# Performance work log

Measured on AMD Instinct MI355X. Metric: run time of the kernel, lower is better.

Reference implementation:

```python
import jax, jax.numpy as jnp
import numpy as np
import math

N_HEADS = 16
EMBED = 1024
D_KEY = EMBED // N_HEADS
B, S = 2, 2048
NEG = -1000000000.0


def setup_inputs() -> dict:
    key = jax.random.key(0)
    ks = jax.random.split(key, 7)
    scale = 1.0 / math.sqrt(EMBED)
    x = jax.random.normal(ks[0], (B, S, EMBED), dtype=jnp.float32)
    Wq_w = jax.random.uniform(ks[1], (EMBED, EMBED), jnp.float32, -scale, scale)
    Wq_b = jax.random.uniform(ks[2], (EMBED,), jnp.float32, -scale, scale)
    Wk_w = jax.random.uniform(ks[3], (EMBED, EMBED), jnp.float32, -scale, scale)
    Wk_b = jax.random.uniform(ks[4], (EMBED,), jnp.float32, -scale, scale)
    Wv_w = jax.random.uniform(ks[5], (EMBED, EMBED), jnp.float32, -scale, scale)
    Wv_b = jax.random.uniform(ks[6], (EMBED,), jnp.float32, -scale, scale)
    return {"x": x, "Wq_w": Wq_w, "Wq_b": Wq_b, "Wk_w": Wk_w, "Wk_b": Wk_b,
            "Wv_w": Wv_w, "Wv_b": Wv_b, "is_masked": 1}


def reference(x, Wq_w, Wq_b, Wk_w, Wk_b, Wv_w, Wv_b, is_masked):
    b, s, e = x.shape
    # nn.Linear: y = x @ W.T + b
    q = x @ Wq_w.T + Wq_b
    k = x @ Wk_w.T + Wk_b
    v = x @ Wv_w.T + Wv_b
    # [B, H, S, Dk]
    q = q.reshape(b, s, N_HEADS, D_KEY).transpose(0, 2, 1, 3)
    k = k.reshape(b, s, N_HEADS, D_KEY).transpose(0, 2, 1, 3)
    v = v.reshape(b, s, N_HEADS, D_KEY).transpose(0, 2, 1, 3)
    scores = jnp.einsum("bhqd,bhkd->bhqk", q, k) / math.sqrt(D_KEY)
    # non-standard mask: keep positions where score != padding (0)
    mask = scores != 0.0
    if is_masked:
        causal = jnp.tril(jnp.ones((1, s, s), dtype=bool))  # broadcasts over B,H
        mask = causal[None] & mask  # [1,1,S,S] & [B,H,S,S]
    scores = jnp.where(mask, scores, NEG)
    probs = jax.nn.softmax(scores, axis=-1)
    out = jnp.einsum("bhqk,bhkd->bhqd", probs, v)
    return out.transpose(0, 2, 1, 3).reshape(b, s, e)
```

## Files before the change

kernel.cpp:

```cpp
#include <hip/hip_runtime.h>

#define B_SZ   2
#define NH     16
#define S_LEN  2048
#define DK     64
#define EMB    1024
#define M_TOT  (B_SZ * S_LEN)
#define KT     64

typedef float          f32x4  __attribute__((ext_vector_type(4)));
typedef float          f32x16 __attribute__((ext_vector_type(16)));
typedef unsigned int   u32x4  __attribute__((ext_vector_type(4)));
typedef unsigned short u16x8  __attribute__((ext_vector_type(8)));
typedef unsigned short u16x4  __attribute__((ext_vector_type(4)));
typedef __bf16         bf16x8 __attribute__((ext_vector_type(8)));

static __device__ __forceinline__ f32x4 mfma16(u16x8 a, u16x8 b, f32x4 c) {
    return __builtin_amdgcn_mfma_f32_16x16x32_bf16(
        __builtin_bit_cast(bf16x8, a), __builtin_bit_cast(bf16x8, b), c, 0, 0, 0);
}
static __device__ __forceinline__ f32x16 mfma32(u16x8 a, u16x8 b, f32x16 c) {
    return __builtin_amdgcn_mfma_f32_32x32x16_bf16(
        __builtin_bit_cast(bf16x8, a), __builtin_bit_cast(bf16x8, b), c, 0, 0, 0);
}

static __device__ __forceinline__ unsigned short f2bf(float f) {
    unsigned int u = __builtin_bit_cast(unsigned int, f);
    u = (u + 0x7FFFu + ((u >> 16) & 1u)) >> 16;
    return (unsigned short)u;
}

static __device__ __forceinline__ float exp2_hw(float x) {
    float r; asm("v_exp_f32 %0, %1" : "=v"(r) : "v"(x)); return r;
}

#define GLDS16(g, l)  __builtin_amdgcn_global_load_lds(                      \
    (const void __attribute__((address_space(1)))*)(g),                      \
    (void __attribute__((address_space(3)))*)(l), 16, 0, 0)

__global__ __launch_bounds__(256) void cvt_kernel(
    const float* __restrict__ x,  const float* __restrict__ wq,
    const float* __restrict__ wk, const float* __restrict__ wv,
    unsigned short* __restrict__ xb,  unsigned short* __restrict__ wqb,
    unsigned short* __restrict__ wkb, unsigned short* __restrict__ wvb)
{
    long gid = (long)blockIdx.x * 256 + threadIdx.x;
    long e = gid * 4;
    const float* src; unsigned short* dst; long off;
    if      (e < 4194304L) { src = x;  dst = xb;  off = e; }
    else if (e < 5242880L) { src = wq; dst = wqb; off = e - 4194304L; }
    else if (e < 6291456L) { src = wk; dst = wkb; off = e - 5242880L; }
    else                   { src = wv; dst = wvb; off = e - 6291456L; }
    f32x4 v = *(const f32x4*)(src + off);
    u16x4 u;
    u[0] = f2bf(v[0]); u[1] = f2bf(v[1]); u[2] = f2bf(v[2]); u[3] = f2bf(v[3]);
    *(u16x4*)(dst + off) = u;
}

#define BM 128
#define BN 128
#define BK 64

__global__ __launch_bounds__(256) void qkv_gemm(
    const unsigned short* __restrict__ xb,
    const unsigned short* __restrict__ wb,
    const float* __restrict__ bq, const float* __restrict__ bk,
    const float* __restrict__ bv,
    unsigned short* __restrict__ qkv)
{
    const int tid  = threadIdx.x;
    const int lane = tid & 63;
    const int wid  = tid >> 6;
    const int wm   = wid >> 1, wn = wid & 1;
    const int n0   = blockIdx.x * BN;
    const int m0   = blockIdx.y * BM;
    const int mat  = blockIdx.z;

    const unsigned short* wmat = wb + (size_t)mat * (1024 * 1024);
    const float* bias = (mat == 0) ? bq : ((mat == 1) ? bk : bv);
    unsigned short* dst = qkv + (size_t)mat * ((size_t)M_TOT * EMB);

    __shared__ __align__(16) unsigned short Al[BM * 64];
    __shared__ __align__(16) unsigned short Bl[BN * 64];

    f32x4 acc[4][4];
#pragma unroll
    for (int i = 0; i < 4; ++i)
#pragma unroll
        for (int j = 0; j < 4; ++j)
            acc[i][j] = (f32x4){0.f, 0.f, 0.f, 0.f};

    const int wrow = wid * 32;
    const int lrow = lane >> 3;
    const int lcol = ((lane & 7) ^ lrow) * 8;
    const int l15  = lane & 15;
    const int sl0 = (((lane >> 4))     ^ (l15 & 7)) * 8;
    const int sl1 = ((4 + (lane >> 4)) ^ (l15 & 7)) * 8;

    for (int k0 = 0; k0 < EMB; k0 += BK) {
        const unsigned short* ga = xb   + (size_t)(m0 + wrow + lrow) * EMB + k0 + lcol;
        const unsigned short* gb = wmat + (size_t)(n0 + wrow + lrow) * EMB + k0 + lcol;
#pragma unroll
        for (int j = 0; j < 4; ++j) {
            GLDS16(ga + (size_t)j * 8 * EMB, &Al[(wrow + j * 8) * 64]);
            GLDS16(gb + (size_t)j * 8 * EMB, &Bl[(wrow + j * 8) * 64]);
        }
        __syncthreads();

#pragma unroll
        for (int kk = 0; kk < 2; ++kk) {
            const int sl = kk ? sl1 : sl0;
            u16x8 a[4], b[4];
#pragma unroll
            for (int i = 0; i < 4; ++i)
                a[i] = *(const u16x8*)&Al[(wm * 64 + i * 16 + l15) * 64 + sl];
#pragma unroll
            for (int j = 0; j < 4; ++j)
                b[j] = *(const u16x8*)&Bl[(wn * 64 + j * 16 + l15) * 64 + sl];
#pragma unroll
            for (int i = 0; i < 4; ++i)
#pragma unroll
                for (int j = 0; j < 4; ++j)
                    acc[i][j] = mfma16(a[i], b[j], acc[i][j]);
        }
        __syncthreads();
    }

#pragma unroll
    for (int j = 0; j < 4; ++j) {
        int n = n0 + wn * 64 + j * 16 + l15;
        float bvv = bias[n];
        int h = n >> 6, d = n & 63;
#pragma unroll
        for (int i = 0; i < 4; ++i) {
#pragma unroll
            for (int r = 0; r < 4; ++r) {
                int m = m0 + wm * 64 + i * 16 + ((lane >> 4) << 2) + r;
                int bb = m >> 11, s = m & 2047;
                dst[((size_t)((bb * NH + h) * S_LEN + s)) * DK + d] =
                    f2bf(acc[i][j][r] + bvv);
            }
        }
    }
}

__global__ __launch_bounds__(512) void attn_kernel(
    const unsigned short* __restrict__ Q,
    const unsigned short* __restrict__ K,
    const unsigned short* __restrict__ V,
    const int* __restrict__ mskp,
    float* __restrict__ out)
{
    const int tid = threadIdx.x, lane = tid & 63, wid = tid >> 6;
    const int grp = wid >> 2, qw = wid & 3;
    const int l31 = lane & 31, H = lane >> 5;
    const int bh = blockIdx.x;
    const int h  = bh & 15, b = bh >> 4;
    const int y  = blockIdx.y;
    const int qt = (y < 8) ? y : 23 - y;
    const int q0 = qt * 128;
    const size_t hoff = ((size_t)(b * NH + h)) * S_LEN * DK;
    const unsigned short* Qh = Q + hoff;
    const unsigned short* Kh = K + hoff;
    const unsigned short* Vh = V + hoff;
    const int msk = *mskp;
    const int ntiles = msk ? (2 * qt + 2) : (S_LEN / KT);
    const int niter  = ntiles >> 1;

    __shared__ __align__(16) unsigned short Kl[2][64 * 64];
    __shared__ __align__(16) unsigned short Vt[2][64 * 64];
    __shared__ float MLbuf[512];
    unsigned short* Kg = Kl[grp];
    unsigned short* Vg = Vt[grp];

    const int qrow = q0 + qw * 32 + l31;
    u16x8 qf[4];
#pragma unroll
    for (int ks = 0; ks < 4; ++ks)
        qf[ks] = *(const u16x8*)(Qh + (size_t)qrow * DK + ks * 16 + H * 8);

    f32x16 o0, o1;
#pragma unroll
    for (int i = 0; i < 16; ++i) { o0[i] = 0.f; o1[i] = 0.f; }
    float mx = -1e30f, lsum = 0.f;

    const int gt  = tid & 255;
    const int sr0 = gt >> 3, sc8 = gt & 7, sr1 = sr0 + 32;
    const int kwo0 = sr0 * 64 + ((sc8 ^ (sr0 & 7)) << 3);
    const int kwo1 = sr1 * 64 + ((sc8 ^ (sr1 & 7)) << 3);
    const int vwo0 = (((sr0 >> 3) ^ sc8) << 3) + (sr0 & 7);
    const int vwo1 = (((sr1 >> 3) ^ sc8) << 3) + (sr1 & 7);

    u16x8 kr[2], vr[2];
    {
        const unsigned short* K0 = Kh + (size_t)grp * KT * DK;
        const unsigned short* V0 = Vh + (size_t)grp * KT * DK;
        kr[0] = *(const u16x8*)(K0 + (size_t)sr0 * DK + sc8 * 8);
        vr[0] = *(const u16x8*)(V0 + (size_t)sr0 * DK + sc8 * 8);
        kr[1] = *(const u16x8*)(K0 + (size_t)sr1 * DK + sc8 * 8);
        vr[1] = *(const u16x8*)(V0 + (size_t)sr1 * DK + sc8 * 8);
    }

    const int qmin = q0 + qw * 32;
    const int dsw0 = l31 >> 3, dsw1 = 4 + (l31 >> 3);
    const int rsw  = l31 & 7;
    const float SC2 = 0.125f * 1.4426950408889634f;

    for (int it = 0; it < niter; ++it) {
        const int kt = 2 * it + grp;
        __syncthreads();
        *(u16x8*)&Kg[kwo0] = kr[0];
        *(u16x8*)&Kg[kwo1] = kr[1];
#pragma unroll
        for (int e = 0; e < 8; ++e) {
            Vg[(sc8 * 8 + e) * 64 + vwo0] = vr[0][e];
            Vg[(sc8 * 8 + e) * 64 + vwo1] = vr[1][e];
        }
        __syncthreads();

        if (it + 1 < niter) {
            const unsigned short* Kn = Kh + (size_t)(kt + 2) * KT * DK;
            const unsigned short* Vn = Vh + (size_t)(kt + 2) * KT * DK;
            kr[0] = *(const u16x8*)(Kn + (size_t)sr0 * DK + sc8 * 8);
            vr[0] = *(const u16x8*)(Vn + (size_t)sr0 * DK + sc8 * 8);
            kr[1] = *(const u16x8*)(Kn + (size_t)sr1 * DK + sc8 * 8);
            vr[1] = *(const u16x8*)(Vn + (size_t)sr1 * DK + sc8 * 8);
        }

        if (msk && kt * KT > qmin + 31) continue;

        f32x16 st0, st1;
#pragma unroll
        for (int i = 0; i < 16; ++i) { st0[i] = 0.f; st1[i] = 0.f; }
        __builtin_amdgcn_s_setprio(1);
#pragma unroll
        for (int ks = 0; ks < 4; ++ks) {
            const int g = (((ks << 1) + H) ^ rsw) << 3;
            u16x8 kf0 = *(const u16x8*)&Kg[l31 * 64 + g];
            u16x8 kf1 = *(const u16x8*)&Kg[(32 + l31) * 64 + g];
            st0 = mfma32(kf0, qf[ks], st0);
            st1 = mfma32(kf1, qf[ks], st1);
        }
        __builtin_amdgcn_s_setprio(0);

        const bool needmask = msk && (kt * KT + 63 > qrow);
        float p[32];
#pragma unroll
        for (int r = 0; r < 16; ++r) {
            const int krow = (r & 3) + 8 * (r >> 2) + 4 * H;
            float v0 = st0[r] * SC2;
            float v1 = st1[r] * SC2;
            if (needmask) {
                if (kt * KT + krow > qrow)      v0 = -1e30f;
                if (kt * KT + 32 + krow > qrow) v1 = -1e30f;
            }
            p[r] = v0; p[16 + r] = v1;
        }

        float t8[8];
#pragma unroll
        for (int i = 0; i < 8; ++i)
            t8[i] = fmaxf(fmaxf(p[i], p[i + 8]), fmaxf(p[i + 16], p[i + 24]));
#pragma unroll
        for (int i = 0; i < 4; ++i) t8[i] = fmaxf(t8[i], t8[i + 4]);
        float mt = fmaxf(fmaxf(t8[0], t8[1]), fmaxf(t8[2], t8[3]));
        mt = fmaxf(mt, __shfl_xor(mt, 32, 64));

        if (!__all(mt <= mx + 11.54f)) {
            const float mn = fmaxf(mx, mt);
            const float al = exp2_hw(mx - mn);
            mx = mn;
            lsum *= al;
#pragma unroll
            for (int i = 0; i < 16; ++i) { o0[i] *= al; o1[i] *= al; }
        }

        float s8[8];
#pragma unroll
        for (int i = 0; i < 8; ++i) s8[i] = 0.f;
#pragma unroll
        for (int r = 0; r < 32; ++r) {
            p[r] = exp2_hw(p[r] - mx);
            s8[r & 7] += p[r];
        }
        float ls = ((s8[0] + s8[1]) + (s8[2] + s8[3])) +
                   ((s8[4] + s8[5]) + (s8[6] + s8[7]));
        ls += __shfl_xor(ls, 32, 64);
        lsum += ls;

        __builtin_amdgcn_s_setprio(1);
#pragma unroll
        for (int ks = 0; ks < 4; ++ks) {
            const int bb = ks * 8;
            unsigned int wa, wb2, wc, wd;
            asm("v_cvt_pk_bf16_f32 %0, %1, %2" : "=v"(wa)  : "v"(p[bb + 0]), "v"(p[bb + 1]));
            asm("v_cvt_pk_bf16_f32 %0, %1, %2" : "=v"(wb2) : "v"(p[bb + 2]), "v"(p[bb + 3]));
            asm("v_cvt_pk_bf16_f32 %0, %1, %2" : "=v"(wc)  : "v"(p[bb + 4]), "v"(p[bb + 5]));
            asm("v_cvt_pk_bf16_f32 %0, %1, %2" : "=v"(wd)  : "v"(p[bb + 6]), "v"(p[bb + 7]));
            asm volatile("v_permlane32_swap_b32 %0, %1" : "+v"(wa),  "+v"(wc));
            asm volatile("v_permlane32_swap_b32 %0, %1" : "+v"(wb2), "+v"(wd));
            u32x4 wv; wv[0] = wa; wv[1] = wb2; wv[2] = wc; wv[3] = wd;
            const u16x8 pb = __builtin_bit_cast(u16x8, wv);
            const int kg = (ks << 1) + H;
            u16x8 vf0 = *(const u16x8*)&Vg[l31 * 64        + ((kg ^ dsw0) << 3)];
            u16x8 vf1 = *(const u16x8*)&Vg[(32 + l31) * 64 + ((kg ^ dsw1) << 3)];
            o0 = mfma32(vf0, pb, o0);
            o1 = mfma32(vf1, pb, o1);
        }
        __builtin_amdgcn_s_setprio(0);
    }

    const int idx = qw * 64 + lane;
    float* MO = (idx < 128) ? ((float*)Kl + idx * 32)
                            : ((float*)Vt + (idx - 128) * 32);
    __syncthreads();
    if (grp == 1) {
#pragma unroll
        for (int i = 0; i < 16; ++i) {
            MO[(i + idx) & 31]      = o0[i];
            MO[(16 + i + idx) & 31] = o1[i];
        }
        MLbuf[idx * 2]     = mx;
        MLbuf[idx * 2 + 1] = lsum;
    }
    __syncthreads();
    if (grp == 0) {
        const float m2 = MLbuf[idx * 2], l2 = MLbuf[idx * 2 + 1];
        const float mn = fmaxf(mx, m2);
        const float ea = exp2_hw(mx - mn);
        const float eb = exp2_hw(m2 - mn);
        const float inv = 1.f / (lsum * ea + l2 * eb);
        float* orow = out + ((size_t)(b * S_LEN) + qrow) * EMB + h * DK;
#pragma unroll
        for (int g = 0; g < 4; ++g) {
            f32x4 w0, w1;
#pragma unroll
            for (int i = 0; i < 4; ++i) {
                w0[i] = (o0[4 * g + i] * ea + MO[(4 * g + i + idx) & 31] * eb) * inv;
                w1[i] = (o1[4 * g + i] * ea + MO[(16 + 4 * g + i + idx) & 31] * eb) * inv;
            }
            *(f32x4*)&orow[8 * g + 4 * H]      = w0;
            *(f32x4*)&orow[32 + 8 * g + 4 * H] = w1;
        }
    }
}

extern "C" void kernel_launch(void* const* d_in, const int* in_sizes, int n_in,
                              void* d_out, int out_size, void* d_ws, size_t ws_size,
                              hipStream_t stream)
{
    const float* x  = (const float*)d_in[0];
    const float* wq = (const float*)d_in[1];
    const float* bq = (const float*)d_in[2];
    const float* wk = (const float*)d_in[3];
    const float* bk = (const float*)d_in[4];
    const float* wv = (const float*)d_in[5];
    const float* bv = (const float*)d_in[6];
    const int* msk  = (const int*)d_in[7];
    float* out = (float*)d_out;

    unsigned short* xb  = (unsigned short*)d_ws;
    unsigned short* wb  = xb + (size_t)M_TOT * EMB;
    unsigned short* qkv = wb + (size_t)3 * 1024 * 1024;

    cvt_kernel<<<7168, 256, 0, stream>>>(x, wq, wk, wv,
                                         xb, wb, wb + 1024 * 1024, wb + 2 * 1024 * 1024);
    qkv_gemm<<<dim3(8, 32, 3), 256, 0, stream>>>(xb, wb, bq, bk, bv, qkv);
    attn_kernel<<<dim3(32, 16, 1), 512, 0, stream>>>(
        qkv, qkv + (size_t)M_TOT * EMB, qkv + (size_t)2 * M_TOT * EMB, msk, out);
}
```

Before: 95.98 us.

## Double-buffer K/V LDS tiles and compute row sums via MFMA with ones

Doubles the LDS buffers for K and V so that the next tile is written into the alternate buffer while the current one is consumed. This removes one of the two block barriers per iteration. The softmax row sum is now accumulated by an extra MFMA that multiplies a ones vector with the bf16 probabilities, replacing the scalar add tree and cross-lane shuffle. In exchange, LDS use doubles, which may lower occupancy, and each iteration issues four extra MFMAs. The row sum is also taken from bf16-rounded probabilities, which changes its numerics slightly.

```diff
diff --git a/kernel.cpp b/kernel.cpp
--- a/kernel.cpp
+++ b/kernel.cpp
@@ -167,11 +167,9 @@
     const int ntiles = msk ? (2 * qt + 2) : (S_LEN / KT);
     const int niter  = ntiles >> 1;
 
-    __shared__ __align__(16) unsigned short Kl[2][64 * 64];
-    __shared__ __align__(16) unsigned short Vt[2][64 * 64];
+    __shared__ __align__(16) unsigned short Kl[2][2][64 * 64];
+    __shared__ __align__(16) unsigned short Vt[2][2][64 * 64];
     __shared__ float MLbuf[512];
-    unsigned short* Kg = Kl[grp];
-    unsigned short* Vg = Vt[grp];
 
     const int qrow = q0 + qw * 32 + l31;
     u16x8 qf[4];
@@ -179,10 +177,14 @@
     for (int ks = 0; ks < 4; ++ks)
         qf[ks] = *(const u16x8*)(Qh + (size_t)qrow * DK + ks * 16 + H * 8);
 
-    f32x16 o0, o1;
-#pragma unroll
-    for (int i = 0; i < 16; ++i) { o0[i] = 0.f; o1[i] = 0.f; }
-    float mx = -1e30f, lsum = 0.f;
+    u16x8 ones1;
+#pragma unroll
+    for (int i = 0; i < 8; ++i) ones1[i] = 0x3F80;
+
+    f32x16 o0, o1, lacc;
+#pragma unroll
+    for (int i = 0; i < 16; ++i) { o0[i] = 0.f; o1[i] = 0.f; lacc[i] = 0.f; }
+    float mx = -1e30f;
 
     const int gt  = tid & 255;
     const int sr0 = gt >> 3, sc8 = gt & 7, sr1 = sr0 + 32;
@@ -190,6 +192,11 @@
     const int kwo1 = sr1 * 64 + ((sc8 ^ (sr1 & 7)) << 3);
     const int vwo0 = (((sr0 >> 3) ^ sc8) << 3) + (sr0 & 7);
     const int vwo1 = (((sr1 >> 3) ^ sc8) << 3) + (sr1 & 7);
+
+    const int qmin = q0 + qw * 32;
+    const int dsw0 = l31 >> 3, dsw1 = 4 + (l31 >> 3);
+    const int rsw  = l31 & 7;
+    const float SC2 = 0.125f * 1.4426950408889634f;
 
     u16x8 kr[2], vr[2];
     {
@@ -199,16 +206,8 @@
         vr[0] = *(const u16x8*)(V0 + (size_t)sr0 * DK + sc8 * 8);
         kr[1] = *(const u16x8*)(K0 + (size_t)sr1 * DK + sc8 * 8);
         vr[1] = *(const u16x8*)(V0 + (size_t)sr1 * DK + sc8 * 8);
-    }
-
-    const int qmin = q0 + qw * 32;
-    const int dsw0 = l31 >> 3, dsw1 = 4 + (l31 >> 3);
-    const int rsw  = l31 & 7;
-    const float SC2 = 0.125f * 1.4426950408889634f;
-
-    for (int it = 0; it < niter; ++it) {
-        const int kt = 2 * it + grp;
-        __syncthreads();
+        unsigned short* Kg = Kl[grp][0];
+        unsigned short* Vg = Vt[grp][0];
         *(u16x8*)&Kg[kwo0] = kr[0];
         *(u16x8*)&Kg[kwo1] = kr[1];
 #pragma unroll
@@ -216,104 +215,124 @@
             Vg[(sc8 * 8 + e) * 64 + vwo0] = vr[0][e];
             Vg[(sc8 * 8 + e) * 64 + vwo1] = vr[1][e];
         }
-        __syncthreads();
-
-        if (it + 1 < niter) {
-            const unsigned short* Kn = Kh + (size_t)(kt + 2) * KT * DK;
-            const unsigned short* Vn = Vh + (size_t)(kt + 2) * KT * DK;
+        if (grp + 2 < ntiles) {
+            const unsigned short* Kn = Kh + (size_t)(grp + 2) * KT * DK;
+            const unsigned short* Vn = Vh + (size_t)(grp + 2) * KT * DK;
             kr[0] = *(const u16x8*)(Kn + (size_t)sr0 * DK + sc8 * 8);
             vr[0] = *(const u16x8*)(Vn + (size_t)sr0 * DK + sc8 * 8);
             kr[1] = *(const u16x8*)(Kn + (size_t)sr1 * DK + sc8 * 8);
             vr[1] = *(const u16x8*)(Vn + (size_t)sr1 * DK + sc8 * 8);
         }
-
-        if (msk && kt * KT > qmin + 31) continue;
-
-        f32x16 st0, st1;
-#pragma unroll
-        for (int i = 0; i < 16; ++i) { st0[i] = 0.f; st1[i] = 0.f; }
-        __builtin_amdgcn_s_setprio(1);
-#pragma unroll
-        for (int ks = 0; ks < 4; ++ks) {
-            const int g = (((ks << 1) + H) ^ rsw) << 3;
-            u16x8 kf0 = *(const u16x8*)&Kg[l31 * 64 + g];
-            u16x8 kf1 = *(const u16x8*)&Kg[(32 + l31) * 64 + g];
-            st0 = mfma32(kf0, qf[ks], st0);
-            st1 = mfma32(kf1, qf[ks], st1);
-        }
-        __builtin_amdgcn_s_setprio(0);
-
-        const bool needmask = msk && (kt * KT + 63 > qrow);
-        float p[32];
-#pragma unroll
-        for (int r = 0; r < 16; ++r) {
-            const int krow = (r & 3) + 8 * (r >> 2) + 4 * H;
-            float v0 = st0[r] * SC2;
-            float v1 = st1[r] * SC2;
+    }
+    __syncthreads();
+
+    int cur = 0;
+    for (int it = 0; it < niter; ++it) {
+        const int kt = 2 * it + grp;
+
+        if (kt + 2 < ntiles) {
+            unsigned short* Kg = Kl[grp][cur ^ 1];
+            unsigned short* Vg = Vt[grp][cur ^ 1];
+            *(u16x8*)&Kg[kwo0] = kr[0];
+            *(u16x8*)&Kg[kwo1] = kr[1];
+#pragma unroll
+            for (int e = 0; e < 8; ++e) {
+                Vg[(sc8 * 8 + e) * 64 + vwo0] = vr[0][e];
+                Vg[(sc8 * 8 + e) * 64 + vwo1] = vr[1][e];
+            }
+        }
+        if (kt + 4 < ntiles) {
+            const unsigned short* Kn = Kh + (size_t)(kt + 4) * KT * DK;
+            const unsigned short* Vn = Vh + (size_t)(kt + 4) * KT * DK;
+            kr[0] = *(const u16x8*)(Kn + (size_t)sr0 * DK + sc8 * 8);
+            vr[0] = *(const u16x8*)(Vn + (size_t)sr0 * DK + sc8 * 8);
+            kr[1] = *(const u16x8*)(Kn + (size_t)sr1 * DK + sc8 * 8);
+            vr[1] = *(const u16x8*)(Vn + (size_t)sr1 * DK + sc8 * 8);
+        }
+
+        if (!(msk && kt * KT > qmin + 31)) {
+            const unsigned short* Kg = Kl[grp][cur];
+            const unsigned short* Vg = Vt[grp][cur];
+
+            f32x16 st0, st1;
+#pragma unroll
+            for (int i = 0; i < 16; ++i) { st0[i] = 0.f; st1[i] = 0.f; }
+            __builtin_amdgcn_s_setprio(1);
+#pragma unroll
+            for (int ks = 0; ks < 4; ++ks) {
+                const int g = (((ks << 1) + H) ^ rsw) << 3;
+                u16x8 kf0 = *(const u16x8*)&Kg[l31 * 64 + g];
+                u16x8 kf1 = *(const u16x8*)&Kg[(32 + l31) * 64 + g];
+                st0 = mfma32(kf0, qf[ks], st0);
+                st1 = mfma32(kf1, qf[ks], st1);
+            }
+            __builtin_amdgcn_s_setprio(0);
+
+            st0 *= SC2;
+            st1 *= SC2;
+            float p[32];
+#pragma unroll
+            for (int r = 0; r < 16; ++r) { p[r] = st0[r]; p[16 + r] = st1[r]; }
+            const bool needmask = msk && (kt * KT + 63 > qrow);
             if (needmask) {
-                if (kt * KT + krow > qrow)      v0 = -1e30f;
-                if (kt * KT + 32 + krow > qrow) v1 = -1e30f;
-            }
-            p[r] = v0; p[16 + r] = v1;
-        }
-
-        float t8[8];
-#pragma unroll
-        for (int i = 0; i < 8; ++i)
-            t8[i] = fmaxf(fmaxf(p[i], p[i + 8]), fmaxf(p[i + 16], p[i + 24]));
-#pragma unroll
-        for (int i = 0; i < 4; ++i) t8[i] = fmaxf(t8[i], t8[i + 4]);
-        float mt = fmaxf(fmaxf(t8[0], t8[1]), fmaxf(t8[2], t8[3]));
-        mt = fmaxf(mt, __shfl_xor(mt, 32, 64));
-
-        if (!__all(mt <= mx + 11.54f)) {
-            const float mn = fmaxf(mx, mt);
-            const float al = exp2_hw(mx - mn);
-            mx = mn;
-            lsum *= al;
-#pragma unroll
-            for (int i = 0; i < 16; ++i) { o0[i] *= al; o1[i] *= al; }
-        }
-
-        float s8[8];
-#pragma unroll
-        for (int i = 0; i < 8; ++i) s8[i] = 0.f;
-#pragma unroll
-        for (int r = 0; r < 32; ++r) {
-            p[r] = exp2_hw(p[r] - mx);
-            s8[r & 7] += p[r];
-        }
-        float ls = ((s8[0] + s8[1]) + (s8[2] + s8[3])) +
-                   ((s8[4] + s8[5]) + (s8[6] + s8[7]));
-        ls += __shfl_xor(ls, 32, 64);
-        lsum += ls;
-
-        __builtin_amdgcn_s_setprio(1);
-#pragma unroll
-        for (int ks = 0; ks < 4; ++ks) {
-            const int bb = ks * 8;
-            unsigned int wa, wb2, wc, wd;
-            asm("v_cvt_pk_bf16_f32 %0, %1, %2" : "=v"(wa)  : "v"(p[bb + 0]), "v"(p[bb + 1]));
-            asm("v_cvt_pk_bf16_f32 %0, %1, %2" : "=v"(wb2) : "v"(p[bb + 2]), "v"(p[bb + 3]));
-            asm("v_cvt_pk_bf16_f32 %0, %1, %2" : "=v"(wc)  : "v"(p[bb + 4]), "v"(p[bb + 5]));
-            asm("v_cvt_pk_bf16_f32 %0, %1, %2" : "=v"(wd)  : "v"(p[bb + 6]), "v"(p[bb + 7]));
-            asm volatile("v_permlane32_swap_b32 %0, %1" : "+v"(wa),  "+v"(wc));
-            asm volatile("v_permlane32_swap_b32 %0, %1" : "+v"(wb2), "+v"(wd));
-            u32x4 wv; wv[0] = wa; wv[1] = wb2; wv[2] = wc; wv[3] = wd;
-            const u16x8 pb = __builtin_bit_cast(u16x8, wv);
-            const int kg = (ks << 1) + H;
-            u16x8 vf0 = *(const u16x8*)&Vg[l31 * 64        + ((kg ^ dsw0) << 3)];
-            u16x8 vf1 = *(const u16x8*)&Vg[(32 + l31) * 64 + ((kg ^ dsw1) << 3)];
-            o0 = mfma32(vf0, pb, o0);
-            o1 = mfma32(vf1, pb, o1);
-        }
-        __builtin_amdgcn_s_setprio(0);
+#pragma unroll
+                for (int r = 0; r < 16; ++r) {
+                    const int krow = (r & 3) + 8 * (r >> 2) + 4 * H;
+                    if (kt * KT + krow > qrow)      p[r]      = -1e30f;
+                    if (kt * KT + 32 + krow > qrow) p[16 + r] = -1e30f;
+                }
+            }
+
+            float t8[8];
+#pragma unroll
+            for (int i = 0; i < 8; ++i)
+                t8[i] = fmaxf(fmaxf(p[i], p[i + 8]), fmaxf(p[i + 16], p[i + 24]));
+#pragma unroll
+            for (int i = 0; i < 4; ++i) t8[i] = fmaxf(t8[i], t8[i + 4]);
+            float mt = fmaxf(fmaxf(t8[0], t8[1]), fmaxf(t8[2], t8[3]));
+            mt = fmaxf(mt, __shfl_xor(mt, 32, 64));
+
+            if (!__all(mt <= mx + 11.54f)) {
+                const float mn = fmaxf(mx, mt);
+                const float al = exp2_hw(mx - mn);
+                mx = mn;
+                o0 *= al; o1 *= al;
+                lacc[0] *= al;
+            }
+
+#pragma unroll
+            for (int r = 0; r < 32; ++r) p[r] = exp2_hw(p[r] - mx);
+
+            __builtin_amdgcn_s_setprio(1);
+#pragma unroll
+            for (int ks = 0; ks < 4; ++ks) {
+                const int bb = ks * 8;
+                unsigned int wa, wb2, wc, wd;
+                asm("v_cvt_pk_bf16_f32 %0, %1, %2" : "=v"(wa)  : "v"(p[bb + 0]), "v"(p[bb + 1]));
+                asm("v_cvt_pk_bf16_f32 %0, %1, %2" : "=v"(wb2) : "v"(p[bb + 2]), "v"(p[bb + 3]));
+                asm("v_cvt_pk_bf16_f32 %0, %1, %2" : "=v"(wc)  : "v"(p[bb + 4]), "v"(p[bb + 5]));
+                asm("v_cvt_pk_bf16_f32 %0, %1, %2" : "=v"(wd)  : "v"(p[bb + 6]), "v"(p[bb + 7]));
+                asm volatile("v_permlane32_swap_b32 %0, %1" : "+v"(wa),  "+v"(wc));
+                asm volatile("v_permlane32_swap_b32 %0, %1" : "+v"(wb2), "+v"(wd));
+                u32x4 wv; wv[0] = wa; wv[1] = wb2; wv[2] = wc; wv[3] = wd;
+                const u16x8 pb = __builtin_bit_cast(u16x8, wv);
+                const int kg = (ks << 1) + H;
+                u16x8 vf0 = *(const u16x8*)&Vg[l31 * 64        + ((kg ^ dsw0) << 3)];
+                u16x8 vf1 = *(const u16x8*)&Vg[(32 + l31) * 64 + ((kg ^ dsw1) << 3)];
+                o0 = mfma32(vf0, pb, o0);
+                o1 = mfma32(vf1, pb, o1);
+                lacc = mfma32(ones1, pb, lacc);
+            }
+            __builtin_amdgcn_s_setprio(0);
+        }
+
+        __syncthreads();
+        cur ^= 1;
     }
 
     const int idx = qw * 64 + lane;
-    float* MO = (idx < 128) ? ((float*)Kl + idx * 32)
-                            : ((float*)Vt + (idx - 128) * 32);
-    __syncthreads();
+    float* MO = (float*)Kl + idx * 32;
+    const float lsum = lacc[0];
     if (grp == 1) {
 #pragma unroll
         for (int i = 0; i < 16; ++i) {
```

After: 91.77 us. 1.05x faster.
